# Performance work log

Measured on AMD Instinct MI355X. Metric: run time of the kernel, lower is better.

Reference implementation:

```python
import jax, jax.numpy as jnp
import numpy as np

D_IN, D_H, D_OUT = 1024, 1024, 1024
D_MOE = 4096
N_EXPERTS = 8
TOP_K = 2


def setup_inputs() -> dict:
    key = jax.random.key(0)
    ks = jax.random.split(key, 10)
    s = lambda d: 1.0 / np.sqrt(d)
    x = jax.random.normal(ks[0], (2, 2048, D_IN), dtype=jnp.float32)
    W_in = jax.random.normal(ks[1], (D_IN, D_H), dtype=jnp.float32) * s(D_IN)
    b_in = jnp.zeros((D_H,), jnp.float32)
    W_gate = jax.random.normal(ks[2], (D_H, N_EXPERTS), dtype=jnp.float32) * s(D_H)
    b_gate = jnp.zeros((N_EXPERTS,), jnp.float32)
    W1 = jax.random.normal(ks[3], (N_EXPERTS, D_H, D_MOE), dtype=jnp.float32) * s(D_H)
    b1 = jnp.zeros((N_EXPERTS, D_MOE), jnp.float32)
    W2 = jax.random.normal(ks[4], (N_EXPERTS, D_MOE, D_H), dtype=jnp.float32) * s(D_MOE)
    b2 = jnp.zeros((N_EXPERTS, D_H), jnp.float32)
    W_out = jax.random.normal(ks[5], (D_H, D_OUT), dtype=jnp.float32) * s(D_H)
    b_out = jnp.zeros((D_OUT,), jnp.float32)
    return {"x": x, "W_in": W_in, "b_in": b_in, "W_gate": W_gate, "b_gate": b_gate,
            "W1": W1, "b1": b1, "W2": W2, "b2": b2, "W_out": W_out, "b_out": b_out}


def reference(x, W_in, b_in, W_gate, b_gate, W1, b1, W2, b2, W_out, b_out):
    B, S, _ = x.shape
    h = x @ W_in + b_in                       # [B,S,D_H]
    t = h.reshape(B * S, -1)                  # tokens [N,D_H]

    # --- top-k softmax gating ---
    logits = t @ W_gate + b_gate              # [N,E]
    probs = jax.nn.softmax(logits, axis=-1)
    topv, topi = jax.lax.top_k(probs, TOP_K)  # [N,k]
    topv = topv / jnp.sum(topv, axis=-1, keepdims=True)
    # dense routing weights [N,E] (zeros for unselected experts)
    route = jnp.zeros_like(probs).at[jnp.arange(t.shape[0])[:, None], topi].set(topv)

    # --- expert MLPs (dense all-expert compute, weighted combine) ---
    mid = jax.nn.relu(jnp.einsum('nd,edh->neh', t, W1) + b1)   # [N,E,D_MOE]
    eout = jnp.einsum('neh,ehd->ned', mid, W2) + b2            # [N,E,D_H]
    moe_out = jnp.einsum('ne,ned->nd', route, eout)            # [N,D_H]

    out = moe_out.reshape(B, S, -1) @ W_out + b_out            # [B,S,D_OUT]
    return out
```

## Files before the change

### kernel.cpp

```cpp
#include <hip/hip_runtime.h>
#include <hip/hip_bf16.h>

typedef __bf16 bf16_t;
typedef bf16_t bf16x8 __attribute__((ext_vector_type(8)));
typedef bf16_t bf16x4 __attribute__((ext_vector_type(4)));
typedef float f32x4 __attribute__((ext_vector_type(4)));

#define DIN 1024
#define DH 1024
#define DMOE 4096
#define NEXP 8
#define NTOK 4096

__device__ __forceinline__ void gload_lds16(const bf16_t* g, bf16_t* l) {
  __builtin_amdgcn_global_load_lds(
      (const __attribute__((address_space(1))) void*)g,
      (__attribute__((address_space(3))) void*)l, 16, 0, 0);
}


__global__ void k_zero8(int* p) {
  if (threadIdx.x < 8) p[threadIdx.x] = 0;
}

__global__ void k_transpose_cvt(const float* __restrict__ src, bf16_t* __restrict__ dst,
                                int R, int C) {
  __shared__ float tile[32][33];
  const size_t mofs = (size_t)blockIdx.z * R * C;
  const float* s = src + mofs;
  bf16_t* d = dst + mofs;
  const int c0 = blockIdx.x * 32, r0 = blockIdx.y * 32;
  const int tx = threadIdx.x, ty = threadIdx.y;
#pragma unroll
  for (int i = 0; i < 32; i += 8)
    tile[ty + i][tx] = s[(size_t)(r0 + ty + i) * C + (c0 + tx)];
  __syncthreads();
#pragma unroll
  for (int i = 0; i < 32; i += 8)
    d[(size_t)(c0 + ty + i) * R + (r0 + tx)] = (bf16_t)tile[tx][ty + i];
}

__global__ void k_cvt_bf16(const float* __restrict__ src, bf16_t* __restrict__ dst, int n4) {
  const int i = blockIdx.x * blockDim.x + threadIdx.x;
  if (i < n4) {
    const float4 v = *(const float4*)(src + (size_t)i * 4);
    bf16x4 o;
    o.x = (bf16_t)v.x; o.y = (bf16_t)v.y; o.z = (bf16_t)v.z; o.w = (bf16_t)v.w;
    *(bf16x4*)(dst + (size_t)i * 4) = o;
  }
}

__global__ void k_gate_prep(const float* __restrict__ Win, const float* __restrict__ Wgate,
                            const float* __restrict__ b_in, const float* __restrict__ b_gate,
                            double* __restrict__ G, double* __restrict__ cvec) {
  const int lane = threadIdx.x & 63;
  const int wave = (blockIdx.x * blockDim.x + threadIdx.x) >> 6;
  const int nw = (gridDim.x * blockDim.x) >> 6;
  for (int d = wave; d <= DIN; d += nw) {
    const float* row = (d < DIN) ? (Win + (size_t)d * DH) : b_in;
    double acc[8] = {0, 0, 0, 0, 0, 0, 0, 0};
    for (int k = lane; k < DH; k += 64) {
      const double xv = (double)row[k];
      const float* g = Wgate + (size_t)k * NEXP;
#pragma unroll
      for (int ee = 0; ee < 8; ++ee) acc[ee] += xv * (double)g[ee];
    }
#pragma unroll
    for (int ee = 0; ee < 8; ++ee) {
      double a = acc[ee];
      for (int o = 32; o > 0; o >>= 1) a += __shfl_down(a, o);
      acc[ee] = a;
    }
    if (lane == 0) {
      if (d < DIN) {
#pragma unroll
        for (int ee = 0; ee < 8; ++ee) G[(size_t)d * 8 + ee] = acc[ee];
      } else {
#pragma unroll
        for (int ee = 0; ee < 8; ++ee) cvec[ee] = acc[ee] + (double)b_gate[ee];
      }
    }
  }
}

__global__ void k_gating(const float* __restrict__ x, const double* __restrict__ G,
                         const double* __restrict__ cvec, int* __restrict__ cnt,
                         int* __restrict__ list, float* __restrict__ wlist) {
  const int lane = threadIdx.x & 63;
  const int t = blockIdx.x * (blockDim.x >> 6) + (threadIdx.x >> 6);
  if (t >= NTOK) return;
  const float* xr = x + (size_t)t * DIN;
  double acc[8] = {0, 0, 0, 0, 0, 0, 0, 0};
  for (int d = lane; d < DIN; d += 64) {
    const double xv = (double)xr[d];
    const double* g = G + (size_t)d * 8;
#pragma unroll
    for (int ee = 0; ee < 8; ++ee) acc[ee] += xv * g[ee];
  }
#pragma unroll
  for (int ee = 0; ee < 8; ++ee) {
    double a = acc[ee];
    for (int o = 32; o > 0; o >>= 1) a += __shfl_down(a, o);
    acc[ee] = a;
  }
  if (lane == 0) {
    double l[8];
#pragma unroll
    for (int ee = 0; ee < 8; ++ee) l[ee] = acc[ee] + cvec[ee];
    double m = l[0];
#pragma unroll
    for (int ee = 1; ee < 8; ++ee) m = fmax(m, l[ee]);
    double p[8];
#pragma unroll
    for (int ee = 0; ee < 8; ++ee) p[ee] = exp(l[ee] - m);
    int i1 = 0;
#pragma unroll
    for (int ee = 1; ee < 8; ++ee)
      if (p[ee] > p[i1]) i1 = ee;
    int i2 = (i1 == 0) ? 1 : 0;
#pragma unroll
    for (int ee = 0; ee < 8; ++ee)
      if (ee != i1 && p[ee] > p[i2]) i2 = ee;
    const double s2 = p[i1] + p[i2];
    const float w1 = (float)(p[i1] / s2);
    const float w2 = (float)(p[i2] / s2);
    int lp = atomicAdd(&cnt[i1], 1);
    list[i1 * NTOK + lp] = t * 2;
    wlist[i1 * NTOK + lp] = w1;
    lp = atomicAdd(&cnt[i2], 1);
    list[i2 * NTOK + lp] = t * 2 + 1;
    wlist[i2 * NTOK + lp] = w2;
  }
}

__global__ void k_scan(const int* __restrict__ cnt, int* __restrict__ offs) {
  if (threadIdx.x == 0) {
    int s = 0;
    for (int e = 0; e < NEXP; ++e) { offs[e] = s; s += cnt[e]; }
    offs[NEXP] = s;
  }
}

__global__ void k_combine(const float* __restrict__ eout, bf16_t* __restrict__ moebf) {
  const int i = blockIdx.x * blockDim.x + threadIdx.x;
  const int t = i >> 8;
  const int q = (i & 255) * 4;
  const float4 a = *(const float4*)(eout + ((size_t)t * 2) * DH + q);
  const float4 b = *(const float4*)(eout + ((size_t)t * 2 + 1) * DH + q);
  bf16x4 o;
  o.x = (bf16_t)(a.x + b.x); o.y = (bf16_t)(a.y + b.y);
  o.z = (bf16_t)(a.z + b.z); o.w = (bf16_t)(a.w + b.w);
  *(bf16x4*)(moebf + (size_t)t * DH + q) = o;
}

template <int MODE>
__global__ __launch_bounds__(256, 3) void k_gemm(
    const bf16_t* __restrict__ Abase, const bf16_t* __restrict__ Bbase,
    const float* __restrict__ biasBase, void* __restrict__ Cbase,
    int M, int N, int K,
    const int* __restrict__ cnt, const int* __restrict__ offs,
    const int* __restrict__ listBase, const float* __restrict__ wlistBase) {
  const int e = blockIdx.z;
  const int hw = blockIdx.y * gridDim.x + blockIdx.x;
  const int lid = (hw & 7) * (gridDim.x << 2) + (hw >> 3);
  const int nblk = lid >> 5;
  const int mblk = lid & 31;
  int Mloc = M;
  const bf16_t* A = Abase;
  const bf16_t* B = Bbase;
  const float* bias = biasBase;
  const int* myList = nullptr;
  const float* myW = nullptr;
  int rowOff = 0;
  if constexpr (MODE == 1 || MODE == 2) {
    Mloc = cnt[e];
    if (mblk * 128 >= Mloc) return;
    B = Bbase + (size_t)e * N * K;
    bias = biasBase + (size_t)e * N;
    myList = listBase + e * NTOK;
    myW = wlistBase + e * NTOK;
    rowOff = offs[e];
    if constexpr (MODE == 2) A = Abase + (size_t)rowOff * K;
  }

  __shared__ bf16_t As[3][128 * 32];
  __shared__ bf16_t Bs[3][128 * 32];

  const int tid = threadIdx.x;
  const int lane = tid & 63;
  const int wid = tid >> 6;
  const int wr = wid >> 1, wc = wid & 1;

  const int srow0 = wid * 32 + (lane >> 2);
  const int srow1 = srow0 + 16;
  const int skcol = (lane & 3) * 8;

  int ar0 = mblk * 128 + srow0;
  int ar1 = mblk * 128 + srow1;
  if constexpr (MODE == 1 || MODE == 2) {
    if (ar0 > Mloc - 1) ar0 = Mloc - 1;
    if (ar1 > Mloc - 1) ar1 = Mloc - 1;
  }
  size_t arow0 = (size_t)ar0, arow1 = (size_t)ar1;
  if constexpr (MODE == 1) {
    arow0 = (size_t)(myList[ar0] >> 1);
    arow1 = (size_t)(myList[ar1] >> 1);
  }
  const bf16_t* aptr0 = A + arow0 * K + skcol;
  const bf16_t* aptr1 = A + arow1 * K + skcol;
  const bf16_t* bptr0 = B + (size_t)(nblk * 128 + srow0) * K + skcol;
  const bf16_t* bptr1 = B + (size_t)(nblk * 128 + srow1) * K + skcol;

  const int ldsOfsA0 = (wid * 32) * 32;
  const int ldsOfsA1 = (wid * 32 + 16) * 32;

  f32x4 acc[4][4] = {};

  const int nkt = K >> 5;

  auto stage = [&](int buf, int kt) {
    const size_t ko = (size_t)kt * 32;
    gload_lds16(aptr0 + ko, &As[buf][ldsOfsA0]);
    gload_lds16(aptr1 + ko, &As[buf][ldsOfsA1]);
    gload_lds16(bptr0 + ko, &Bs[buf][ldsOfsA0]);
    gload_lds16(bptr1 + ko, &Bs[buf][ldsOfsA1]);
  };

  stage(0, 0);
  if (nkt > 1) stage(1, 1);

  int cur = 0;
  for (int kt = 0; kt < nkt; ++kt) {
    int nxt = cur + 2;
    if (nxt >= 3) nxt -= 3;
    if (kt + 2 < nkt) {
      stage(nxt, kt + 2);
      asm volatile("s_waitcnt vmcnt(8)" ::: "memory");
    } else if (kt + 1 < nkt) {
      asm volatile("s_waitcnt vmcnt(4)" ::: "memory");
    } else {
      asm volatile("s_waitcnt vmcnt(0)" ::: "memory");
    }
    __builtin_amdgcn_s_barrier();

    const int fr = lane & 15;
    const int kq = (lane >> 4) * 8;
    bf16x8 af[4], bfr[4];
#pragma unroll
    for (int m = 0; m < 4; ++m)
      af[m] = *(const bf16x8*)&As[cur][(wr * 64 + m * 16 + fr) * 32 + kq];
#pragma unroll
    for (int n = 0; n < 4; ++n)
      bfr[n] = *(const bf16x8*)&Bs[cur][(wc * 64 + n * 16 + fr) * 32 + kq];
    __builtin_amdgcn_s_setprio(1);
#pragma unroll
    for (int m = 0; m < 4; ++m)
#pragma unroll
      for (int n = 0; n < 4; ++n)
        acc[m][n] = __builtin_amdgcn_mfma_f32_16x16x32_bf16(af[m], bfr[n], acc[m][n], 0, 0, 0);
    __builtin_amdgcn_s_setprio(0);

    __builtin_amdgcn_s_barrier();
    cur += 1;
    if (cur >= 3) cur -= 3;
  }

  const int colBase = nblk * 128 + wc * 64 + (lane & 15);
  const int rowBase = mblk * 128 + wr * 64 + ((lane >> 4) << 2);
#pragma unroll
  for (int n = 0; n < 4; ++n) {
    const int c = colBase + n * 16;
    const float bv = bias[c];
#pragma unroll
    for (int m = 0; m < 4; ++m) {
#pragma unroll
      for (int j = 0; j < 4; ++j) {
        const int r = rowBase + m * 16 + j;
        float v = acc[m][n][j] + bv;
        if constexpr (MODE == 0) {
          ((bf16_t*)Cbase)[(size_t)r * N + c] = (bf16_t)v;
        } else if constexpr (MODE == 1) {
          if (r < Mloc) {
            v = fmaxf(v, 0.0f);
            ((bf16_t*)Cbase)[(size_t)(rowOff + r) * N + c] = (bf16_t)v;
          }
        } else if constexpr (MODE == 2) {
          if (r < Mloc) {
            const int entry = myList[r];
            const float w = myW[r];
            ((float*)Cbase)[(size_t)entry * DH + c] = v * w;
          }
        } else {
          ((float*)Cbase)[(size_t)r * N + c] = v;
        }
      }
    }
  }
}


extern "C" void kernel_launch(void* const* d_in, const int* in_sizes, int n_in,
                              void* d_out, int out_size, void* d_ws, size_t ws_size,
                              hipStream_t stream) {
  const float* x      = (const float*)d_in[0];
  const float* W_in   = (const float*)d_in[1];
  const float* b_in   = (const float*)d_in[2];
  const float* W_gate = (const float*)d_in[3];
  const float* b_gate = (const float*)d_in[4];
  const float* W1     = (const float*)d_in[5];
  const float* b1     = (const float*)d_in[6];
  const float* W2     = (const float*)d_in[7];
  const float* b2     = (const float*)d_in[8];
  const float* W_out  = (const float*)d_in[9];
  const float* b_out  = (const float*)d_in[10];

  char* ws = (char*)d_ws;
  size_t off = 0;
  auto alloc = [&](size_t bytes) -> void* {
    void* p = ws + off;
    off += (bytes + 255) & ~(size_t)255;
    return p;
  };

  bf16_t* WtIn  = (bf16_t*)alloc((size_t)DH * DIN * 2);
  bf16_t* Wt1   = (bf16_t*)alloc((size_t)NEXP * DMOE * DH * 2);
  bf16_t* Wt2   = (bf16_t*)alloc((size_t)NEXP * DH * DMOE * 2);
  bf16_t* WtOut = (bf16_t*)alloc((size_t)DH * DH * 2);
  bf16_t* xbf   = (bf16_t*)alloc((size_t)NTOK * DIN * 2);
  bf16_t* hbf   = (bf16_t*)alloc((size_t)NTOK * DH * 2);
  bf16_t* mid   = (bf16_t*)alloc((size_t)2 * NTOK * DMOE * 2);
  float*  eout  = (float*)alloc((size_t)2 * NTOK * DH * 4);
  bf16_t* moebf = (bf16_t*)alloc((size_t)NTOK * DH * 2);
  double* G     = (double*)alloc((size_t)DIN * 8 * 8);
  double* cvec  = (double*)alloc(8 * 8);
  int*    cnt   = (int*)alloc(NEXP * 4);
  int*    offs  = (int*)alloc((NEXP + 1) * 4);
  int*    list  = (int*)alloc((size_t)NEXP * NTOK * 4);
  float*  wlist = (float*)alloc((size_t)NEXP * NTOK * 4);

  k_zero8<<<1, 64, 0, stream>>>(cnt);

  dim3 tb(32, 8, 1);
  k_transpose_cvt<<<dim3(DH / 32, DIN / 32, 1), tb, 0, stream>>>(W_in, WtIn, DIN, DH);
  k_transpose_cvt<<<dim3(DMOE / 32, DH / 32, NEXP), tb, 0, stream>>>(W1, Wt1, DH, DMOE);
  k_transpose_cvt<<<dim3(DH / 32, DMOE / 32, NEXP), tb, 0, stream>>>(W2, Wt2, DMOE, DH);
  k_transpose_cvt<<<dim3(DH / 32, DH / 32, 1), tb, 0, stream>>>(W_out, WtOut, DH, DH);
  k_cvt_bf16<<<(NTOK * DIN / 4 + 255) / 256, 256, 0, stream>>>(x, xbf, NTOK * DIN / 4);

  k_gate_prep<<<64, 256, 0, stream>>>(W_in, W_gate, b_in, b_gate, G, cvec);
  k_gating<<<NTOK / 4, 256, 0, stream>>>(x, G, cvec, cnt, list, wlist);
  k_scan<<<1, 64, 0, stream>>>(cnt, offs);

  k_gemm<0><<<dim3(DH / 128, NTOK / 128, 1), 256, 0, stream>>>(
      xbf, WtIn, b_in, hbf, NTOK, DH, DIN, nullptr, nullptr, nullptr, nullptr);
  k_gemm<1><<<dim3(DMOE / 128, NTOK / 128, NEXP), 256, 0, stream>>>(
      hbf, Wt1, b1, mid, NTOK, DMOE, DH, cnt, offs, list, wlist);
  k_gemm<2><<<dim3(DH / 128, NTOK / 128, NEXP), 256, 0, stream>>>(
      mid, Wt2, b2, eout, NTOK, DH, DMOE, cnt, offs, list, wlist);
  k_combine<<<NTOK * DH / 4 / 256, 256, 0, stream>>>(eout, moebf);
  k_gemm<3><<<dim3(DH / 128, NTOK / 128, 1), 256, 0, stream>>>(
      moebf, WtOut, b_out, (float*)d_out, NTOK, DH, DH, nullptr, nullptr, nullptr, nullptr);
}
```

Measured before the change: 611.4 us.

## Enlarge GEMM tiles to 256x256 with 8 waves, swizzled LDS and interleaved prefetch

Rewrites the shared GEMM kernel to use 256x256 output tiles with 512 threads and a K-step of 64. It adds an XOR-swizzled LDS layout and splits each K-step into two halves, so global-to-LDS prefetches are interleaved with MFMA issue under explicit waitcnt and sched_barrier control. The grid remap now derives tile indices from gridDim rather than hardcoded constants, and the expert GEMM grids are sized for 2*NTOK rows. Each tile gets more data reuse and fewer tiles are launched, but the larger tiles raise register and LDS pressure and waste more work on partial expert tiles.

```diff
diff --git a/kernel.cpp b/kernel.cpp
--- a/kernel.cpp
+++ b/kernel.cpp
@@ -154,17 +154,20 @@
 }
 
 template <int MODE>
-__global__ __launch_bounds__(256, 3) void k_gemm(
+__global__ __launch_bounds__(512, 2) void k_gemm(
     const bf16_t* __restrict__ Abase, const bf16_t* __restrict__ Bbase,
     const float* __restrict__ biasBase, void* __restrict__ Cbase,
     int M, int N, int K,
     const int* __restrict__ cnt, const int* __restrict__ offs,
     const int* __restrict__ listBase, const float* __restrict__ wlistBase) {
   const int e = blockIdx.z;
+  const int mtiles = gridDim.y;
   const int hw = blockIdx.y * gridDim.x + blockIdx.x;
-  const int lid = (hw & 7) * (gridDim.x << 2) + (hw >> 3);
-  const int nblk = lid >> 5;
-  const int mblk = lid & 31;
+  const int cpx = (gridDim.x * gridDim.y) >> 3;
+  const int lid = (hw & 7) * cpx + (hw >> 3);
+  const int mblk = lid % mtiles;
+  const int nblk = lid / mtiles;
+
   int Mloc = M;
   const bf16_t* A = Abase;
   const bf16_t* B = Bbase;
@@ -174,7 +177,7 @@
   int rowOff = 0;
   if constexpr (MODE == 1 || MODE == 2) {
     Mloc = cnt[e];
-    if (mblk * 128 >= Mloc) return;
+    if (mblk * 256 >= Mloc) return;
     B = Bbase + (size_t)e * N * K;
     bias = biasBase + (size_t)e * N;
     myList = listBase + e * NTOK;
@@ -183,96 +186,145 @@
     if constexpr (MODE == 2) A = Abase + (size_t)rowOff * K;
   }
 
-  __shared__ bf16_t As[3][128 * 32];
-  __shared__ bf16_t Bs[3][128 * 32];
+  __shared__ bf16_t As[4 * 128 * 64];
+  __shared__ bf16_t Bs[4 * 128 * 64];
 
   const int tid = threadIdx.x;
   const int lane = tid & 63;
   const int wid = tid >> 6;
-  const int wr = wid >> 1, wc = wid & 1;
-
-  const int srow0 = wid * 32 + (lane >> 2);
-  const int srow1 = srow0 + 16;
-  const int skcol = (lane & 3) * 8;
-
-  int ar0 = mblk * 128 + srow0;
-  int ar1 = mblk * 128 + srow1;
-  if constexpr (MODE == 1 || MODE == 2) {
-    if (ar0 > Mloc - 1) ar0 = Mloc - 1;
-    if (ar1 > Mloc - 1) ar1 = Mloc - 1;
-  }
-  size_t arow0 = (size_t)ar0, arow1 = (size_t)ar1;
-  if constexpr (MODE == 1) {
-    arow0 = (size_t)(myList[ar0] >> 1);
-    arow1 = (size_t)(myList[ar1] >> 1);
-  }
-  const bf16_t* aptr0 = A + arow0 * K + skcol;
-  const bf16_t* aptr1 = A + arow1 * K + skcol;
-  const bf16_t* bptr0 = B + (size_t)(nblk * 128 + srow0) * K + skcol;
-  const bf16_t* bptr1 = B + (size_t)(nblk * 128 + srow1) * K + skcol;
-
-  const int ldsOfsA0 = (wid * 32) * 32;
-  const int ldsOfsA1 = (wid * 32 + 16) * 32;
-
-  f32x4 acc[4][4] = {};
-
-  const int nkt = K >> 5;
-
-  auto stage = [&](int buf, int kt) {
-    const size_t ko = (size_t)kt * 32;
-    gload_lds16(aptr0 + ko, &As[buf][ldsOfsA0]);
-    gload_lds16(aptr1 + ko, &As[buf][ldsOfsA1]);
-    gload_lds16(bptr0 + ko, &Bs[buf][ldsOfsA0]);
-    gload_lds16(bptr1 + ko, &Bs[buf][ldsOfsA1]);
+  const int wr = wid >> 2;
+  const int wcn = wid & 3;
+
+  const int sub_r = lane >> 3;
+  const int colg = ((lane & 7) ^ sub_r) * 8;
+  uint32_t aoff[2][2], boff[2][2];
+#pragma unroll
+  for (int h = 0; h < 2; ++h) {
+#pragma unroll
+    for (int l = 0; l < 2; ++l) {
+      const int c = wid * 2 + l;
+      int ar = mblk * 256 + h * 128 + c * 8 + sub_r;
+      const int br = nblk * 256 + h * 128 + c * 8 + sub_r;
+      if constexpr (MODE == 1 || MODE == 2) {
+        if (ar > Mloc - 1) ar = Mloc - 1;
+      }
+      uint32_t arow = (uint32_t)ar;
+      if constexpr (MODE == 1) arow = (uint32_t)(myList[ar] >> 1);
+      aoff[h][l] = arow * (uint32_t)K + colg;
+      boff[h][l] = (uint32_t)br * (uint32_t)K + colg;
+    }
+  }
+
+  auto stageA = [&](int buf, int kt) {
+    const uint32_t ko = (uint32_t)kt * 64;
+#pragma unroll
+    for (int h = 0; h < 2; ++h)
+#pragma unroll
+      for (int l = 0; l < 2; ++l)
+        gload_lds16(A + aoff[h][l] + ko,
+                    &As[(buf * 2 + h) * 8192 + (wid * 2 + l) * 512]);
   };
-
-  stage(0, 0);
-  if (nkt > 1) stage(1, 1);
-
-  int cur = 0;
-  for (int kt = 0; kt < nkt; ++kt) {
-    int nxt = cur + 2;
-    if (nxt >= 3) nxt -= 3;
-    if (kt + 2 < nkt) {
-      stage(nxt, kt + 2);
-      asm volatile("s_waitcnt vmcnt(8)" ::: "memory");
-    } else if (kt + 1 < nkt) {
-      asm volatile("s_waitcnt vmcnt(4)" ::: "memory");
-    } else {
-      asm volatile("s_waitcnt vmcnt(0)" ::: "memory");
-    }
-    __builtin_amdgcn_s_barrier();
-
-    const int fr = lane & 15;
-    const int kq = (lane >> 4) * 8;
-    bf16x8 af[4], bfr[4];
-#pragma unroll
-    for (int m = 0; m < 4; ++m)
-      af[m] = *(const bf16x8*)&As[cur][(wr * 64 + m * 16 + fr) * 32 + kq];
-#pragma unroll
-    for (int n = 0; n < 4; ++n)
-      bfr[n] = *(const bf16x8*)&Bs[cur][(wc * 64 + n * 16 + fr) * 32 + kq];
-    __builtin_amdgcn_s_setprio(1);
-#pragma unroll
-    for (int m = 0; m < 4; ++m)
+  auto stageB = [&](int buf, int kt) {
+    const uint32_t ko = (uint32_t)kt * 64;
+#pragma unroll
+    for (int h = 0; h < 2; ++h)
+#pragma unroll
+      for (int l = 0; l < 2; ++l)
+        gload_lds16(B + boff[h][l] + ko,
+                    &Bs[(buf * 2 + h) * 8192 + (wid * 2 + l) * 512]);
+  };
+
+  const int fr = lane & 15;
+  const int s0 = (((lane >> 4) ^ (fr & 7)) << 3);
+  const bf16_t* Ahalf0 = &As[wr * 8192];
+  const bf16_t* Bhalf0 = &Bs[(wcn >> 1) * 8192];
+  const int brow0 = (wcn & 1) * 64;
+
+  f32x4 acc[8][4] = {};
+
+  const int nkt = K >> 6;
+  const int iters = nkt >> 1;
+
+  stageA(0, 0);
+  stageB(0, 0);
+  stageA(1, 1);
+  stageB(1, 1);
+
+  bf16x8 a0[8], a1[8], b0[4], b1[4];
+
+  for (int it = 0; it < iters; ++it) {
+    const bool prefetch = (it + 1 < iters);
+#pragma unroll
+    for (int half = 0; half < 2; ++half) {
+      if (half == 0 || prefetch) {
+        asm volatile("s_waitcnt vmcnt(8)" ::: "memory");
+      } else {
+        asm volatile("s_waitcnt vmcnt(0)" ::: "memory");
+      }
+      __builtin_amdgcn_s_barrier();
+      const bf16_t* Ah = Ahalf0 + half * 16384;
+      const bf16_t* Bh = Bhalf0 + half * 16384;
+#pragma unroll
+      for (int m = 0; m < 4; ++m) a0[m] = *(const bf16x8*)&Ah[(m * 16 + fr) * 64 + s0];
+#pragma unroll
+      for (int n = 0; n < 4; ++n) b0[n] = *(const bf16x8*)&Bh[(brow0 + n * 16 + fr) * 64 + s0];
+#pragma unroll
+      for (int m = 4; m < 8; ++m) a0[m] = *(const bf16x8*)&Ah[(m * 16 + fr) * 64 + s0];
+      asm volatile("s_waitcnt lgkmcnt(4)" ::: "memory");
+      __builtin_amdgcn_sched_barrier(0);
+      __builtin_amdgcn_s_setprio(1);
+#pragma unroll
+      for (int m = 0; m < 4; ++m)
+#pragma unroll
+        for (int n = 0; n < 4; ++n)
+          acc[m][n] = __builtin_amdgcn_mfma_f32_16x16x32_bf16(a0[m], b0[n], acc[m][n], 0, 0, 0);
+      __builtin_amdgcn_s_setprio(0);
+#pragma unroll
+      for (int m = 0; m < 4; ++m) a1[m] = *(const bf16x8*)&Ah[(m * 16 + fr) * 64 + (s0 ^ 32)];
 #pragma unroll
       for (int n = 0; n < 4; ++n)
-        acc[m][n] = __builtin_amdgcn_mfma_f32_16x16x32_bf16(af[m], bfr[n], acc[m][n], 0, 0, 0);
-    __builtin_amdgcn_s_setprio(0);
-
-    __builtin_amdgcn_s_barrier();
-    cur += 1;
-    if (cur >= 3) cur -= 3;
-  }
-
-  const int colBase = nblk * 128 + wc * 64 + (lane & 15);
-  const int rowBase = mblk * 128 + wr * 64 + ((lane >> 4) << 2);
+        b1[n] = *(const bf16x8*)&Bh[(brow0 + n * 16 + fr) * 64 + (s0 ^ 32)];
+#pragma unroll
+      for (int m = 4; m < 8; ++m) a1[m] = *(const bf16x8*)&Ah[(m * 16 + fr) * 64 + (s0 ^ 32)];
+      asm volatile("s_waitcnt lgkmcnt(12)" ::: "memory");
+      __builtin_amdgcn_sched_barrier(0);
+      __builtin_amdgcn_s_setprio(1);
+#pragma unroll
+      for (int m = 4; m < 8; ++m)
+#pragma unroll
+        for (int n = 0; n < 4; ++n)
+          acc[m][n] = __builtin_amdgcn_mfma_f32_16x16x32_bf16(a0[m], b0[n], acc[m][n], 0, 0, 0);
+      __builtin_amdgcn_s_setprio(0);
+      asm volatile("s_waitcnt lgkmcnt(0)" ::: "memory");
+      __builtin_amdgcn_sched_barrier(0);
+      __builtin_amdgcn_s_barrier();
+      if (prefetch) stageA(half, 2 * it + 2 + half);
+      __builtin_amdgcn_s_setprio(1);
+#pragma unroll
+      for (int m = 0; m < 4; ++m)
+#pragma unroll
+        for (int n = 0; n < 4; ++n)
+          acc[m][n] = __builtin_amdgcn_mfma_f32_16x16x32_bf16(a1[m], b1[n], acc[m][n], 0, 0, 0);
+      __builtin_amdgcn_s_setprio(0);
+      if (prefetch) stageB(half, 2 * it + 2 + half);
+      __builtin_amdgcn_s_setprio(1);
+#pragma unroll
+      for (int m = 4; m < 8; ++m)
+#pragma unroll
+        for (int n = 0; n < 4; ++n)
+          acc[m][n] = __builtin_amdgcn_mfma_f32_16x16x32_bf16(a1[m], b1[n], acc[m][n], 0, 0, 0);
+      __builtin_amdgcn_s_setprio(0);
+    }
+  }
+
+  const int colBase = nblk * 256 + wcn * 64 + (lane & 15);
+  const int rowBase = mblk * 256 + wr * 128 + ((lane >> 4) << 2);
 #pragma unroll
   for (int n = 0; n < 4; ++n) {
     const int c = colBase + n * 16;
     const float bv = bias[c];
 #pragma unroll
-    for (int m = 0; m < 4; ++m) {
+    for (int m = 0; m < 8; ++m) {
 #pragma unroll
       for (int j = 0; j < 4; ++j) {
         const int r = rowBase + m * 16 + j;
@@ -351,13 +403,13 @@
   k_gating<<<NTOK / 4, 256, 0, stream>>>(x, G, cvec, cnt, list, wlist);
   k_scan<<<1, 64, 0, stream>>>(cnt, offs);
 
-  k_gemm<0><<<dim3(DH / 128, NTOK / 128, 1), 256, 0, stream>>>(
+  k_gemm<0><<<dim3(DH / 256, NTOK / 256, 1), 512, 0, stream>>>(
       xbf, WtIn, b_in, hbf, NTOK, DH, DIN, nullptr, nullptr, nullptr, nullptr);
-  k_gemm<1><<<dim3(DMOE / 128, NTOK / 128, NEXP), 256, 0, stream>>>(
-      hbf, Wt1, b1, mid, NTOK, DMOE, DH, cnt, offs, list, wlist);
-  k_gemm<2><<<dim3(DH / 128, NTOK / 128, NEXP), 256, 0, stream>>>(
-      mid, Wt2, b2, eout, NTOK, DH, DMOE, cnt, offs, list, wlist);
+  k_gemm<1><<<dim3(DMOE / 256, 2 * NTOK / 256, NEXP), 512, 0, stream>>>(
+      hbf, Wt1, b1, mid, 2 * NTOK, DMOE, DH, cnt, offs, list, wlist);
+  k_gemm<2><<<dim3(DH / 256, 2 * NTOK / 256, NEXP), 512, 0, stream>>>(
+      mid, Wt2, b2, eout, 2 * NTOK, DH, DMOE, cnt, offs, list, wlist);
   k_combine<<<NTOK * DH / 4 / 256, 256, 0, stream>>>(eout, moebf);
-  k_gemm<3><<<dim3(DH / 128, NTOK / 128, 1), 256, 0, stream>>>(
+  k_gemm<3><<<dim3(DH / 256, NTOK / 256, 1), 512, 0, stream>>>(
       moebf, WtOut, b_out, (float*)d_out, NTOK, DH, DH, nullptr, nullptr, nullptr, nullptr);
 }
```

New measurement: 1.149 ms. +87.9%, slower.
